# Kernel tuning notes

Hardware: AMD Instinct MI355X
Metric: run time of the kernel (lower is better)

## Reference

```python
import jax, jax.numpy as jnp
import numpy as np

B, IN, H, L = 128, 256, 1024, 256
nA, nB = H // 2, (H - 1) // 2        # pairs per A-layer / B-layer
LB = L // 2
LA = L - LB                           # A layers come first when L is odd
PI = float(np.pi)


def setup_inputs() -> dict:
    key = jax.random.key(0)
    ks = jax.random.split(key, 14)
    u = lambda k, shp: jax.random.uniform(k, shp, minval=-PI, maxval=PI)
    return {
        "inputsR": jax.random.normal(ks[0], (B, IN), dtype=jnp.float32),
        "inputsI": jax.random.normal(ks[1], (B, IN), dtype=jnp.float32),
        "stateR": jax.random.normal(ks[2], (B, H), dtype=jnp.float32),
        "stateI": jax.random.normal(ks[3], (B, H), dtype=jnp.float32),
        # CLinear params (init_scale=0.01 inside RNNCellCmplx)
        "weightR": 0.01 * jax.random.normal(ks[4], (H, IN), dtype=jnp.float32),
        "weightI": 0.01 * jax.random.normal(ks[5], (H, IN), dtype=jnp.float32),
        "biasR": 0.01 * jax.random.normal(ks[6], (H,), dtype=jnp.float32),
        "biasI": 0.01 * jax.random.normal(ks[7], (H,), dtype=jnp.float32),
        # Clements mesh angles, uniform(-pi, pi)
        "angleA0": u(ks[8], (LA, nA)),
        "angleA1": u(ks[9], (LA, nA)),
        "angleB0": u(ks[10], (LB, nB)),
        "angleB1": u(ks[11], (LB, nB)),
        # diagonal phase + modReLU bias (both init to zero)
        "omega": jnp.zeros((H,), dtype=jnp.float32),
        "mod_bias": jnp.zeros((H,), dtype=jnp.float32),
    }


def _mzi(ar, ai, br, bi, th0, th1):
    """PSDC MZI on channel pairs: phase shifter e^{i*th0} on arm a, then a
    directional coupler with coupling angle th1 (unitary 2x2)."""
    c0, s0 = jnp.cos(th0), jnp.sin(th0)
    pr = c0 * ar - s0 * ai          # p = e^{i th0} * a
    pi_ = s0 * ar + c0 * ai
    c, s = jnp.cos(th1), jnp.sin(th1)
    oar = c * pr - s * bi           # a' = cos*p + i sin*b
    oai = c * pi_ + s * br
    obr = c * br - s * pi_          # b' = i sin*p + cos*b
    obi = c * bi + s * pr
    return oar, oai, obr, obi


def _layerA(xr, xi, t0, t1):
    Bs, N = xr.shape
    oar, oai, obr, obi = _mzi(xr[:, 0::2], xi[:, 0::2], xr[:, 1::2], xi[:, 1::2], t0, t1)
    xr = jnp.stack([oar, obr], axis=-1).reshape(Bs, N)
    xi = jnp.stack([oai, obi], axis=-1).reshape(Bs, N)
    return xr, xi


def _layerB(xr, xi, t0, t1):
    Bs, N = xr.shape  # pairs (1,2),(3,4),... ; channels 0 and N-1 pass through
    oar, oai, obr, obi = _mzi(xr[:, 1:-1:2], xi[:, 1:-1:2], xr[:, 2::2], xi[:, 2::2], t0, t1)
    midr = jnp.stack([oar, obr], axis=-1).reshape(Bs, N - 2)
    midi = jnp.stack([oai, obi], axis=-1).reshape(Bs, N - 2)
    xr = jnp.concatenate([xr[:, :1], midr, xr[:, -1:]], axis=1)
    xi = jnp.concatenate([xi[:, :1], midi, xi[:, -1:]], axis=1)
    return xr, xi


def _clements(xr, xi, A0, A1, B0, B1):
    def step(carry, ang):
        cr, ci = carry
        a0, a1, b0, b1 = ang
        cr, ci = _layerA(cr, ci, a0, a1)
        cr, ci = _layerB(cr, ci, b0, b1)
        return (cr, ci), None
    (xr, xi), _ = jax.lax.scan(step, (xr, xi), (A0[:LB], A1[:LB], B0, B1))
    for k in range(LB, LA):  # trailing A layer when num_layers is odd (static)
        xr, xi = _layerA(xr, xi, A0[k], A1[k])
    return xr, xi


def _forward(inputsR, inputsI, stateR, stateI, weightR, weightI, biasR, biasI,
             angleA0, angleA1, angleB0, angleB1, omega, mod_bias):
    # CLinear: complex y = W x + b
    ihR = inputsR @ weightR.T - inputsI @ weightI.T + biasR
    ihI = inputsR @ weightI.T + inputsI @ weightR.T + biasI
    # Clements unitary mesh on hidden state
    hr, hi = _clements(stateR, stateI, angleA0, angleA1, angleB0, angleB1)
    # diagonal phase e^{i omega}
    co, so = jnp.cos(omega), jnp.sin(omega)
    hhR = co * hr - so * hi
    hhI = so * hr + co * hi
    # complex add
    zr = ihR + hhR
    zi = ihI + hhI
    # modReLU: relu(|z| + b) * z / |z|
    mag = jnp.sqrt(zr * zr + zi * zi)
    scale = jax.nn.relu(mag + mod_bias) / jnp.maximum(mag, 1e-8)
    return jnp.stack([scale * zr, scale * zi])  # (2, B, H)


def reference(inputsR, inputsI, stateR, stateI, weightR, weightI, biasR, biasI,
              angleA0, angleA1, angleB0, angleB1, omega, mod_bias):
    return _forward(inputsR, inputsI, stateR, stateI, weightR, weightI, biasR, biasI,
                    angleA0, angleA1, angleB0, angleB1, omega, mod_bias)
```

## Files before the change

### kernel.cpp

```cpp
#include <hip/hip_runtime.h>
#include <math.h>

typedef float v2 __attribute__((ext_vector_type(2)));

#define NBATCH 128
#define NIN    256
#define NH     1024
#define NSTEPS 128
#define NB     511

#define TAB_F4_PER_L 1024
#define IH_OFF (NSTEPS * TAB_F4_PER_L * 4)

#define GEMM_BLOCKS 256
#define TRIG_BLOCKS 512

static __device__ __forceinline__ v2 to2(float a, float b) { v2 r; r.x = a; r.y = b; return r; }

__global__ __launch_bounds__(256) void prep_kernel(
    const float* __restrict__ inR, const float* __restrict__ inI,
    const float* __restrict__ wR,  const float* __restrict__ wI,
    const float* __restrict__ biasR, const float* __restrict__ biasI,
    const float* __restrict__ A0, const float* __restrict__ A1,
    const float* __restrict__ B0, const float* __restrict__ B1,
    float* __restrict__ ws)
{
    __shared__ v2 xs[256][17];
    __shared__ v2 wsh[32][34];

    if (blockIdx.x >= GEMM_BLOCKS) {
        int idx = (blockIdx.x - GEMM_BLOCKS) * 256 + threadIdx.x;
        int l = idx >> 10;
        int s = idx & 1023;
        int j = s >> 8, g = s & 255;
        float a0, a1;
        bool ident = false;
        if (j < 2) {
            int p = 2 * g + j;
            a0 = A0[l * 512 + p]; a1 = A1[l * 512 + p];
        } else {
            int p = 2 * g + (j - 2);
            if (p < NB) { a0 = B0[l * NB + p]; a1 = B1[l * NB + p]; }
            else ident = true;
        }
        float4 v;
        if (ident) v = make_float4(1.f, 0.f, 1.f, 0.f);
        else {
            float s0, c0, s1, c1;
            __sincosf(a0, &s0, &c0);
            __sincosf(a1, &s1, &c1);
            v = make_float4(c0, s0, c1, s1);
        }
        ((float4*)ws)[l * TAB_F4_PER_L + j * 256 + g] = v;
        return;
    }

    const int ht = blockIdx.x >> 3, bt = blockIdx.x & 7;
    const int h0 = ht * 32, b0 = bt * 16;
    const int tid = threadIdx.x;

    {
        int b = tid >> 4, k4 = tid & 15;
#pragma unroll
        for (int p = 0; p < 4; ++p) {
            int k0 = p * 64 + k4 * 4;
            float4 vr = *(const float4*)(inR + (b0 + b) * NIN + k0);
            float4 vi = *(const float4*)(inI + (b0 + b) * NIN + k0);
            xs[k0 + 0][b] = to2(vr.x, vi.x);
            xs[k0 + 1][b] = to2(vr.y, vi.y);
            xs[k0 + 2][b] = to2(vr.z, vi.z);
            xs[k0 + 3][b] = to2(vr.w, vi.w);
        }
    }

    const int hg = tid & 15, bl = tid >> 4;
    v2 acc0 = to2(0.f, 0.f), acc1 = to2(0.f, 0.f);

    for (int c = 0; c < 8; ++c) {
        __syncthreads();
        {
            int hh = tid >> 3, k4 = tid & 7;
            float4 vr = *(const float4*)(wR + (h0 + hh) * NIN + c * 32 + k4 * 4);
            float4 vi = *(const float4*)(wI + (h0 + hh) * NIN + c * 32 + k4 * 4);
            wsh[k4 * 4 + 0][hh] = to2(vr.x, vi.x);
            wsh[k4 * 4 + 1][hh] = to2(vr.y, vi.y);
            wsh[k4 * 4 + 2][hh] = to2(vr.z, vi.z);
            wsh[k4 * 4 + 3][hh] = to2(vr.w, vi.w);
        }
        __syncthreads();
#pragma unroll
        for (int k = 0; k < 32; ++k) {
            float4 wv = *(const float4*)&wsh[k][hg * 2];
            v2 w0 = to2(wv.x, wv.y), w1 = to2(wv.z, wv.w);
            v2 xv = xs[c * 32 + k][bl];
            acc0 += to2(xv.x, xv.x) * w0 + to2(xv.y, xv.y) * to2(-w0.y, w0.x);
            acc1 += to2(xv.x, xv.x) * w1 + to2(xv.y, xv.y) * to2(-w1.y, w1.x);
        }
    }
    int h = h0 + hg * 2, b = b0 + bl;
    acc0 += to2(biasR[h], biasI[h]);
    acc1 += to2(biasR[h + 1], biasI[h + 1]);
    ((float4*)(ws + IH_OFF))[b * 512 + (h >> 1)] =
        make_float4(acc0.x, acc0.y, acc1.x, acc1.y);
}

__device__ __forceinline__ void mzi(const float4 t, v2& a, v2& b)
{
    v2 P  = to2(t.x, t.y) * to2(a.x, a.x) + to2(-t.y, t.x) * to2(a.y, a.y);
    v2 na = to2(t.z, t.z) * P + to2(-t.w, t.w) * to2(b.y, b.x);
    b     = to2(t.z, t.z) * b + to2(-t.w, t.w) * to2(P.y, P.x);
    a = na;
}

__device__ __forceinline__ void stepf(v2 x[4], const float4* T, const float4 TL,
                                      int w, int lane, int par,
                                      v2 (&sA0)[2][4], v2 (&sA3)[2][4])
{
    mzi(T[0], x[0], x[1]);
    mzi(T[1], x[2], x[3]);
    float rcr = __shfl_down(x[0].x, 1, 64);
    float rci = __shfl_down(x[0].y, 1, 64);
    float lcr = __shfl_up(x[3].x, 1, 64);
    float lci = __shfl_up(x[3].y, 1, 64);
    if (lane == 0)  sA0[par][w] = x[0];
    if (lane == 63) sA3[par][w] = x[3];
    __syncthreads();
    if (lane == 63 && w < 3) { v2 t = sA0[par][w + 1]; rcr = t.x; rci = t.y; }
    if (lane == 0  && w > 0) { v2 t = sA3[par][w - 1]; lcr = t.x; lci = t.y; }
    mzi(T[2], x[1], x[2]);
    {
        const float4 t = T[3];
        v2 P = to2(t.x, t.y) * to2(x[3].x, x[3].x) + to2(-t.y, t.x) * to2(x[3].y, x[3].y);
        x[3] = to2(t.z, t.z) * P + to2(-t.w, t.w) * to2(rci, rcr);
    }
    {
        v2 P = to2(TL.x, TL.y) * to2(lcr, lcr) + to2(-TL.y, TL.x) * to2(lci, lci);
        x[0] = to2(TL.z, TL.z) * x[0] + to2(-TL.w, TL.w) * to2(P.y, P.x);
    }
}

#define LOADL(T, TL, l)                                                   \
    do {                                                                  \
        const float4* _p = tab + (l) * TAB_F4_PER_L + g;                  \
        T[0] = _p[0];                                                     \
        T[1] = _p[256];                                                   \
        T[2] = _p[512];                                                   \
        T[3] = _p[768];                                                   \
        TL = _p[767];                                     \
        if (g == 0) TL = make_float4(1.f, 0.f, 1.f, 0.f);                 \
    } while (0)

__global__ __launch_bounds__(256, 1) void mesh_kernel(
    const float* __restrict__ stateR, const float* __restrict__ stateI,
    const float* __restrict__ omega,  const float* __restrict__ mod_bias,
    const float* __restrict__ ws, float* __restrict__ out)
{
    const int b = blockIdx.x;
    const int g = threadIdx.x;
    const int lane = g & 63;
    const int w = g >> 6;
    const float4* tab = (const float4*)ws;

    __shared__ v2 sA0[2][4];
    __shared__ v2 sA3[2][4];

    v2 x[4];
    {
        float4 r = *(const float4*)(stateR + b * NH + 4 * g);
        float4 i = *(const float4*)(stateI + b * NH + 4 * g);
        x[0] = to2(r.x, i.x);
        x[1] = to2(r.y, i.y);
        x[2] = to2(r.z, i.z);
        x[3] = to2(r.w, i.w);
    }

    float4 Ta[4], Tb[4], TLa, TLb;
    LOADL(Ta, TLa, 0);
    for (int l = 0; l < NSTEPS; l += 2) {
        LOADL(Tb, TLb, l + 1);
        stepf(x, Ta, TLa, w, lane, 0, sA0, sA3);
        {
            int ln = (l + 2 < NSTEPS) ? l + 2 : NSTEPS - 1;
            LOADL(Ta, TLa, ln);
        }
        stepf(x, Tb, TLb, w, lane, 1, sA0, sA3);
    }

    float4 o4 = *(const float4*)(omega + 4 * g);
    float4 m4 = *(const float4*)(mod_bias + 4 * g);
    const float4* ihp = (const float4*)(ws + IH_OFF) + b * 512 + 2 * g;
    float4 ih0 = ihp[0], ih1 = ihp[1];

    float om[4] = { o4.x, o4.y, o4.z, o4.w };
    float mb[4] = { m4.x, m4.y, m4.z, m4.w };
    float ihr[4] = { ih0.x, ih0.z, ih1.x, ih1.z };
    float ihi[4] = { ih0.y, ih0.w, ih1.y, ih1.w };
    float oR[4], oI[4];
#pragma unroll
    for (int j = 0; j < 4; ++j) {
        float so, co;
        __sincosf(om[j], &so, &co);
        float zr = ihr[j] + co * x[j].x - so * x[j].y;
        float zi = ihi[j] + so * x[j].x + co * x[j].y;
        float mag = sqrtf(zr * zr + zi * zi);
        float sc = fmaxf(mag + mb[j], 0.f) / fmaxf(mag, 1e-8f);
        oR[j] = sc * zr;
        oI[j] = sc * zi;
    }
    *(float4*)(out + b * NH + 4 * g) = make_float4(oR[0], oR[1], oR[2], oR[3]);
    *(float4*)(out + NBATCH * NH + b * NH + 4 * g) = make_float4(oI[0], oI[1], oI[2], oI[3]);
}

extern "C" void kernel_launch(void* const* d_in, const int* in_sizes, int n_in,
                              void* d_out, int out_size, void* d_ws, size_t ws_size,
                              hipStream_t stream)
{
    const float* inputsR = (const float*)d_in[0];
    const float* inputsI = (const float*)d_in[1];
    const float* stateR  = (const float*)d_in[2];
    const float* stateI  = (const float*)d_in[3];
    const float* weightR = (const float*)d_in[4];
    const float* weightI = (const float*)d_in[5];
    const float* biasR   = (const float*)d_in[6];
    const float* biasI   = (const float*)d_in[7];
    const float* angleA0 = (const float*)d_in[8];
    const float* angleA1 = (const float*)d_in[9];
    const float* angleB0 = (const float*)d_in[10];
    const float* angleB1 = (const float*)d_in[11];
    const float* omega   = (const float*)d_in[12];
    const float* mod_b   = (const float*)d_in[13];
    float* ws = (float*)d_ws;
    float* out = (float*)d_out;

    hipLaunchKernelGGL(prep_kernel, dim3(GEMM_BLOCKS + TRIG_BLOCKS), dim3(256),
                       0, stream, inputsR, inputsI, weightR, weightI,
                       biasR, biasI, angleA0, angleA1, angleB0, angleB1, ws);
    hipLaunchKernelGGL(mesh_kernel, dim3(NBATCH), dim3(256), 0, stream,
                       stateR, stateI, omega, mod_b, ws, out);
}
```

Baseline: 151.3 us.

## Replace per-step block barrier with neighbor-wave flag handshakes in mesh kernel

Swaps the __syncthreads in each mesh step for point-to-point synchronization. Each wave writes its boundary values and a step counter flag to LDS, then spin-waits only on its neighbor waves' flags. Independent MZI work is placed between the publish and the wait to hide latency. This removes the full-block barrier, but adds volatile LDS spinning and relies on wave scheduling and memory ordering for correctness. The double-buffered slots indexed by parity also leave some risk of a fast wave overwriting a slot before a slow neighbor has read it.

```diff
diff --git a/kernel.cpp b/kernel.cpp
--- a/kernel.cpp
+++ b/kernel.cpp
@@ -113,21 +113,33 @@
 }
 
 __device__ __forceinline__ void stepf(v2 x[4], const float4* T, const float4 TL,
-                                      int w, int lane, int par,
-                                      v2 (&sA0)[2][4], v2 (&sA3)[2][4])
+                                      int w, int lane, int par, int l,
+                                      volatile float (*vX0)[3][2],
+                                      volatile float (*vX3)[3][2],
+                                      volatile int* fX0, volatile int* fX3)
 {
     mzi(T[0], x[0], x[1]);
     mzi(T[1], x[2], x[3]);
+    if (lane == 0 && w > 0)  { vX0[par][w - 1][0] = x[0].x; vX0[par][w - 1][1] = x[0].y; }
+    if (lane == 63 && w < 3) { vX3[par][w][0] = x[3].x;     vX3[par][w][1] = x[3].y; }
+    __asm__ volatile("s_waitcnt lgkmcnt(0)" ::: "memory");
+    if (lane == 0 && w > 0)  fX0[w - 1] = l + 1;
+    if (lane == 63 && w < 3) fX3[w] = l + 1;
+
     float rcr = __shfl_down(x[0].x, 1, 64);
     float rci = __shfl_down(x[0].y, 1, 64);
     float lcr = __shfl_up(x[3].x, 1, 64);
     float lci = __shfl_up(x[3].y, 1, 64);
-    if (lane == 0)  sA0[par][w] = x[0];
-    if (lane == 63) sA3[par][w] = x[3];
-    __syncthreads();
-    if (lane == 63 && w < 3) { v2 t = sA0[par][w + 1]; rcr = t.x; rci = t.y; }
-    if (lane == 0  && w > 0) { v2 t = sA3[par][w - 1]; lcr = t.x; lci = t.y; }
+
     mzi(T[2], x[1], x[2]);
+
+    if (w == 0)      { while (fX0[0] < l + 1) {} }
+    else if (w == 3) { while (fX3[2] < l + 1) {} }
+    else             { while (fX0[w] < l + 1 || fX3[w - 1] < l + 1) {} }
+
+    if (lane == 63 && w < 3) { rcr = vX0[par][w][0]; rci = vX0[par][w][1]; }
+    if (lane == 0 && w > 0)  { lcr = vX3[par][w - 1][0]; lci = vX3[par][w - 1][1]; }
+
     {
         const float4 t = T[3];
         v2 P = to2(t.x, t.y) * to2(x[3].x, x[3].x) + to2(-t.y, t.x) * to2(x[3].y, x[3].y);
@@ -161,8 +173,16 @@
     const int w = g >> 6;
     const float4* tab = (const float4*)ws;
 
-    __shared__ v2 sA0[2][4];
-    __shared__ v2 sA3[2][4];
+    __shared__ float vX0s[2][3][2];
+    __shared__ float vX3s[2][3][2];
+    __shared__ int fX0s[3], fX3s[3];
+    volatile float (*vX0)[3][2] = vX0s;
+    volatile float (*vX3)[3][2] = vX3s;
+    volatile int* fX0 = fX0s;
+    volatile int* fX3 = fX3s;
+
+    if (g < 3) { fX0s[g] = 0; fX3s[g] = 0; }
+    __syncthreads();
 
     v2 x[4];
     {
@@ -178,12 +198,12 @@
     LOADL(Ta, TLa, 0);
     for (int l = 0; l < NSTEPS; l += 2) {
         LOADL(Tb, TLb, l + 1);
-        stepf(x, Ta, TLa, w, lane, 0, sA0, sA3);
+        stepf(x, Ta, TLa, w, lane, 0, l, vX0, vX3, fX0, fX3);
         {
             int ln = (l + 2 < NSTEPS) ? l + 2 : NSTEPS - 1;
             LOADL(Ta, TLa, ln);
         }
-        stepf(x, Tb, TLb, w, lane, 1, sA0, sA3);
+        stepf(x, Tb, TLb, w, lane, 1, l + 1, vX0, vX3, fX0, fX3);
     }
 
     float4 o4 = *(const float4*)(omega + 4 * g);
```

New measurement: 218.0 us. 1.44x slower.

## Use overlapping halo per wave to replace per-layer block barriers with chunked exchange

Applied to the files above, without the earlier changes.

Each wave now holds an overlapping window of 6 channels per lane, 384 channels per wave including a 64-channel halo on each side. It advances 32 mesh layers using only intra-wave shuffles, then exchanges state through shared memory with one barrier pair per chunk instead of a __syncthreads every layer. The angle table is re-laid out with padding so halo lanes read identity MZIs outside the valid range. This trades about 50% redundant MZI arithmetic and more registers for removing 128 block-wide barriers.

```diff
diff --git a/kernel.cpp b/kernel.cpp
--- a/kernel.cpp
+++ b/kernel.cpp
@@ -8,12 +8,13 @@
 #define NH     1024
 #define NSTEPS 128
 #define NB     511
-
-#define TAB_F4_PER_L 1024
-#define IH_OFF (NSTEPS * TAB_F4_PER_L * 4)
+#define CHUNK  32
+
+#define TAB_STRIDE 1160
+#define IH_OFF (NSTEPS * TAB_STRIDE * 4)
 
 #define GEMM_BLOCKS 256
-#define TRIG_BLOCKS 512
+#define TRIG_BLOCKS 580
 
 static __device__ __forceinline__ v2 to2(float a, float b) { v2 r; r.x = a; r.y = b; return r; }
 
@@ -30,18 +31,18 @@
 
     if (blockIdx.x >= GEMM_BLOCKS) {
         int idx = (blockIdx.x - GEMM_BLOCKS) * 256 + threadIdx.x;
-        int l = idx >> 10;
-        int s = idx & 1023;
-        int j = s >> 8, g = s & 255;
-        float a0, a1;
-        bool ident = false;
-        if (j < 2) {
-            int p = 2 * g + j;
-            a0 = A0[l * 512 + p]; a1 = A1[l * 512 + p];
+        int l = idx / TAB_STRIDE;
+        int i = idx - l * TAB_STRIDE;
+        float a0 = 0.f, a1 = 0.f;
+        bool ident;
+        if (i < 576) {
+            int p = i - 32;
+            ident = (p < 0 || p >= 512);
+            if (!ident) { a0 = A0[l * 512 + p]; a1 = A1[l * 512 + p]; }
         } else {
-            int p = 2 * g + (j - 2);
-            if (p < NB) { a0 = B0[l * NB + p]; a1 = B1[l * NB + p]; }
-            else ident = true;
+            int p = i - 609;
+            ident = (p < 0 || p >= NB);
+            if (!ident) { a0 = B0[l * NB + p]; a1 = B1[l * NB + p]; }
         }
         float4 v;
         if (ident) v = make_float4(1.f, 0.f, 1.f, 0.f);
@@ -51,7 +52,7 @@
             __sincosf(a1, &s1, &c1);
             v = make_float4(c0, s0, c1, s1);
         }
-        ((float4*)ws)[l * TAB_F4_PER_L + j * 256 + g] = v;
+        ((float4*)ws)[l * TAB_STRIDE + i] = v;
         return;
     }
 
@@ -112,42 +113,35 @@
     a = na;
 }
 
-__device__ __forceinline__ void stepf(v2 x[4], const float4* T, const float4 TL,
-                                      int w, int lane, int par,
-                                      v2 (&sA0)[2][4], v2 (&sA3)[2][4])
+__device__ __forceinline__ void stepf(v2 x[6], const float4 T[7])
 {
     mzi(T[0], x[0], x[1]);
     mzi(T[1], x[2], x[3]);
+    mzi(T[2], x[4], x[5]);
     float rcr = __shfl_down(x[0].x, 1, 64);
     float rci = __shfl_down(x[0].y, 1, 64);
-    float lcr = __shfl_up(x[3].x, 1, 64);
-    float lci = __shfl_up(x[3].y, 1, 64);
-    if (lane == 0)  sA0[par][w] = x[0];
-    if (lane == 63) sA3[par][w] = x[3];
-    __syncthreads();
-    if (lane == 63 && w < 3) { v2 t = sA0[par][w + 1]; rcr = t.x; rci = t.y; }
-    if (lane == 0  && w > 0) { v2 t = sA3[par][w - 1]; lcr = t.x; lci = t.y; }
-    mzi(T[2], x[1], x[2]);
+    float lcr = __shfl_up(x[5].x, 1, 64);
+    float lci = __shfl_up(x[5].y, 1, 64);
+    mzi(T[4], x[1], x[2]);
+    mzi(T[5], x[3], x[4]);
+    {
+        const float4 t = T[6];
+        v2 P = to2(t.x, t.y) * to2(x[5].x, x[5].x) + to2(-t.y, t.x) * to2(x[5].y, x[5].y);
+        x[5] = to2(t.z, t.z) * P + to2(-t.w, t.w) * to2(rci, rcr);
+    }
     {
         const float4 t = T[3];
-        v2 P = to2(t.x, t.y) * to2(x[3].x, x[3].x) + to2(-t.y, t.x) * to2(x[3].y, x[3].y);
-        x[3] = to2(t.z, t.z) * P + to2(-t.w, t.w) * to2(rci, rcr);
-    }
-    {
-        v2 P = to2(TL.x, TL.y) * to2(lcr, lcr) + to2(-TL.y, TL.x) * to2(lci, lci);
-        x[0] = to2(TL.z, TL.z) * x[0] + to2(-TL.w, TL.w) * to2(P.y, P.x);
-    }
-}
-
-#define LOADL(T, TL, l)                                                   \
-    do {                                                                  \
-        const float4* _p = tab + (l) * TAB_F4_PER_L + g;                  \
-        T[0] = _p[0];                                                     \
-        T[1] = _p[256];                                                   \
-        T[2] = _p[512];                                                   \
-        T[3] = _p[768];                                                   \
-        TL = _p[767];                                     \
-        if (g == 0) TL = make_float4(1.f, 0.f, 1.f, 0.f);                 \
+        v2 P = to2(t.x, t.y) * to2(lcr, lcr) + to2(-t.y, t.x) * to2(lci, lci);
+        x[0] = to2(t.z, t.z) * x[0] + to2(-t.w, t.w) * to2(P.y, P.x);
+    }
+}
+
+#define LOADT(T, l)                                                        \
+    do {                                                                   \
+        const float4* _a = tab + (l) * TAB_STRIDE + 32 + pa;               \
+        T[0] = _a[0]; T[1] = _a[1]; T[2] = _a[2];                          \
+        const float4* _b = tab + (l) * TAB_STRIDE + 609 + pa;              \
+        T[3] = _b[-1]; T[4] = _b[0]; T[5] = _b[1]; T[6] = _b[2];           \
     } while (0)
 
 __global__ __launch_bounds__(256, 1) void mesh_kernel(
@@ -159,31 +153,57 @@
     const int g = threadIdx.x;
     const int lane = g & 63;
     const int w = g >> 6;
+    const int wb = w * 256;
+    const int cb = wb - 64 + 6 * lane;
+    const int pa = cb / 2;
     const float4* tab = (const float4*)ws;
 
-    __shared__ v2 sA0[2][4];
-    __shared__ v2 sA3[2][4];
-
-    v2 x[4];
-    {
-        float4 r = *(const float4*)(stateR + b * NH + 4 * g);
-        float4 i = *(const float4*)(stateI + b * NH + 4 * g);
-        x[0] = to2(r.x, i.x);
-        x[1] = to2(r.y, i.y);
-        x[2] = to2(r.z, i.z);
-        x[3] = to2(r.w, i.w);
-    }
-
-    float4 Ta[4], Tb[4], TLa, TLb;
-    LOADL(Ta, TLa, 0);
-    for (int l = 0; l < NSTEPS; l += 2) {
-        LOADL(Tb, TLb, l + 1);
-        stepf(x, Ta, TLa, w, lane, 0, sA0, sA3);
-        {
-            int ln = (l + 2 < NSTEPS) ? l + 2 : NSTEPS - 1;
-            LOADL(Ta, TLa, ln);
-        }
-        stepf(x, Tb, TLb, w, lane, 1, sA0, sA3);
+    __shared__ v2 can[NH];
+
+    {
+        float4 r = ((const float4*)(stateR + b * NH))[g];
+        float4 i = ((const float4*)(stateI + b * NH))[g];
+        can[4 * g + 0] = to2(r.x, i.x);
+        can[4 * g + 1] = to2(r.y, i.y);
+        can[4 * g + 2] = to2(r.z, i.z);
+        can[4 * g + 3] = to2(r.w, i.w);
+    }
+    __syncthreads();
+    v2 x[6];
+#pragma unroll
+    for (int j = 0; j < 6; ++j) {
+        int c = cb + j;
+        x[j] = (c >= 0 && c < NH) ? can[c] : to2(0.f, 0.f);
+    }
+    __syncthreads();
+
+    float4 Ta[7], Tb[7];
+    LOADT(Ta, 0);
+    for (int chunk = 0; chunk < 4; ++chunk) {
+        for (int k = 0; k < CHUNK; k += 2) {
+            int l = chunk * CHUNK + k;
+            LOADT(Tb, l + 1);
+            stepf(x, Ta);
+            {
+                int ln = (l + 2 < NSTEPS) ? l + 2 : NSTEPS - 1;
+                LOADT(Ta, ln);
+            }
+            stepf(x, Tb);
+        }
+#pragma unroll
+        for (int j = 0; j < 6; ++j) {
+            int c = cb + j;
+            if (c >= wb && c < wb + 256) can[c] = x[j];
+        }
+        __syncthreads();
+        if (chunk < 3) {
+#pragma unroll
+            for (int j = 0; j < 6; ++j) {
+                int c = cb + j;
+                x[j] = (c >= 0 && c < NH) ? can[c] : to2(0.f, 0.f);
+            }
+            __syncthreads();
+        }
     }
 
     float4 o4 = *(const float4*)(omega + 4 * g);
@@ -198,10 +218,11 @@
     float oR[4], oI[4];
 #pragma unroll
     for (int j = 0; j < 4; ++j) {
+        v2 xx = can[4 * g + j];
         float so, co;
         __sincosf(om[j], &so, &co);
-        float zr = ihr[j] + co * x[j].x - so * x[j].y;
-        float zi = ihi[j] + so * x[j].x + co * x[j].y;
+        float zr = ihr[j] + co * xx.x - so * xx.y;
+        float zi = ihi[j] + so * xx.x + co * xx.y;
         float mag = sqrtf(zr * zr + zi * zi);
         float sc = fmaxf(mag + mb[j], 0.f) / fmaxf(mag, 1e-8f);
         oR[j] = sc * zr;
```

Result: slower. 157.9 us (+4.4%).
